# Optimization experiments

Measured on AMD Instinct MI355X. Metric: run time of the kernel, lower is better.

Reference implementation:

```python
import jax, jax.numpy as jnp
import numpy as np

P_TOP = 0.1          # fraction of brightest pixels for atmosphere
LEC_K = 3            # local-extremum conv kernel size (w=3 in forward)
HID = 64             # hidden channels of stand-in Net


def _conv2d(x, w, pad):
    return jax.lax.conv_general_dilated(
        x, w, window_strides=(1, 1), padding=[(pad, pad), (pad, pad)],
        dimension_numbers=("NCHW", "OIHW", "NCHW"))


def _lec_weights(k, dtype):
    # LocalExtremumConv.init_weights: all +/-1/k^2 with +/-1 at the center
    base = jnp.full((1, 1, k, k), 1.0 / (k * k), dtype=dtype)
    base = base.at[0, 0, k // 2, k // 2].set(1.0)
    return -base, base  # (min_weights, max_weights)


def setup_inputs() -> dict:
    key = jax.random.key(0)
    ks = jax.random.split(key, 8)
    B, C, H, W = 8, 3, 512, 512
    x = jax.random.uniform(ks[0], (B, C, H, W), dtype=jnp.float32)
    s1 = 1.0 / np.sqrt(C * 9)
    s2 = 1.0 / np.sqrt(HID * 9)
    return {
        "x": x,
        "net_w1": jax.random.normal(ks[1], (HID, C, 3, 3), jnp.float32) * s1,
        "net_b1": jnp.zeros((HID,), jnp.float32),
        "net_w2": jax.random.normal(ks[2], (C, HID, 3, 3), jnp.float32) * s2,
        "net_b2": jnp.zeros((C,), jnp.float32),
        "color_w": jax.random.normal(ks[3], (3, 3), jnp.float32) * (1.0 / np.sqrt(3)),
        "color_b": jnp.zeros((3,), jnp.float32),
        "conv_w": jax.random.normal(ks[4], (4, 3, 1, 1), jnp.float32) * (1.0 / np.sqrt(3)),
        "conv_b": jnp.zeros((4,), jnp.float32),
    }


def reference(x, net_w1, net_b1, net_w2, net_b2, color_w, color_b, conv_w, conv_b):
    B, C, H, W = x.shape
    # --- stand-in Net: 3->64->3 conv enhancement, sigmoid output ---
    h = jax.nn.relu(_conv2d(x, net_w1, 1) + net_b1[None, :, None, None])
    img_high = jax.nn.sigmoid(_conv2d(h, net_w2, 1) + net_b2[None, :, None, None])
    # --- stand-in Color_pred: GAP -> linear -> sigmoid -> (B,3,1,1) gain ---
    color = jax.nn.sigmoid(x.mean(axis=(2, 3)) @ color_w.T + color_b)
    img_high = img_high * color[:, :, None, None]
    # --- 1x1 conv -> split K (1ch), Bias (3ch); residual correction ---
    feat = _conv2d(img_high, conv_w, 0) + conv_b[None, :, None, None]
    K, Bt = feat[:, 0:1], feat[:, 1:4]
    x_out = K * x - Bt + x
    # --- illumination channel: reflect pad + channel min/max + LEC convs ---
    pad = LEC_K // 2
    xp = jnp.pad(x_out, ((0, 0), (0, 0), (pad, pad), (pad, pad)), mode="reflect")
    x_max = xp.max(axis=1, keepdims=True)
    _, max_w = _lec_weights(LEC_K, x.dtype)
    bright = jax.nn.relu(_conv2d(x_max, max_w, 0))  # (B,1,H,W)
    # --- atmosphere: top-p% brightest pixels, gather + mean ---
    # NOTE: faithful to torch images.view(B,-1,C) on NCHW (layout-scrambled)
    flat_img = x_out.reshape(B, H * W, C)
    flat_bright = bright.reshape(B, H * W)
    num_pixels = int(P_TOP * H * W)
    _, idx = jax.lax.top_k(flat_bright, num_pixels)          # (B, num_pixels)
    picked = jnp.take_along_axis(flat_img, idx[:, :, None], axis=1)
    A = picked.mean(axis=1)                                   # (B, C)
    return (x_out, A)
```

## Files before the change

kernel.cpp:

```cpp
#include <hip/hip_runtime.h>
#include <hip/hip_bf16.h>

#define Hn 512
#define Wn 512
#define HWn (512 * 512)
#define KTOP 26214

typedef __attribute__((ext_vector_type(8))) short frag_ab;
typedef __attribute__((ext_vector_type(4))) float frag_cd;

__device__ __forceinline__ float sigf(float z) { return 1.0f / (1.0f + __expf(-z)); }

__device__ __forceinline__ short f2bf(float f) {
  unsigned u = __float_as_uint(f);
  u += 0x7FFFu + ((u >> 16) & 1u);
  return (short)(u >> 16);
}

__device__ __forceinline__ unsigned aload(const unsigned* p) {
  return __hip_atomic_load(p, __ATOMIC_RELAXED, __HIP_MEMORY_SCOPE_AGENT);
}

__global__ __launch_bounds__(256) void k_means(
    const float* __restrict__ x, float* __restrict__ means, unsigned* __restrict__ doneCnt,
    const float* __restrict__ w1, const float* __restrict__ b1, const float* __restrict__ w2,
    const float* __restrict__ cw, const float* __restrict__ cb,
    short* __restrict__ w1A, short* __restrict__ w2A, float* __restrict__ colorG)
{
  const int tid = threadIdx.x;
  __shared__ int lastS;
  int bc = blockIdx.x >> 5;
  int slice = blockIdx.x & 31;
  const float4* p = (const float4*)(x + bc * HWn + slice * 8192);
  float s = 0.f;
  for (int i = tid; i < 2048; i += 256) { float4 v = p[i]; s += v.x + v.y + v.z + v.w; }
  for (int off = 32; off > 0; off >>= 1) s += __shfl_down(s, off);
  if ((tid & 63) == 0) atomicAdd(&means[bc], s);
  __syncthreads();
  if (tid == 0) {
    unsigned tk = __hip_atomic_fetch_add(doneCnt, 1u, __ATOMIC_RELAXED, __HIP_MEMORY_SCOPE_AGENT);
    lastS = (tk == 767);
  }
  __syncthreads();
  if (!lastS) return;

  {
    int chunk = tid >> 6, lane = tid & 63;
    int m = lane & 15, q = lane >> 4;
    for (int j = 0; j < 8; ++j) {
      int k = q * 8 + j;
      float v = (k < 27) ? w1[(chunk * 16 + m) * 27 + k] : 0.f;
      w1A[tid * 8 + j] = f2bf(v);
    }
  }
  for (int i = tid; i < 384; i += 256) {
    int step = i >> 6, lane = i & 63;
    int m = lane & 15, q = lane >> 4;
    int dx = step >> 1, half = step & 1;
    int dy = m / 3, oc = m - dy * 3;
    for (int j = 0; j < 8; ++j) {
      int ch = half * 32 + q * 8 + j;
      float v = (m < 9) ? w2[oc * 576 + ch * 9 + dy * 3 + dx] : 0.f;
      w2A[i * 8 + j] = f2bf(v);
    }
  }
  if (tid < 24) {
    int b = tid / 3, oc = tid % 3;
    float z = cb[oc];
    for (int j = 0; j < 3; ++j)
      z += (atomicAdd(&means[b * 3 + j], 0.f) * (1.0f / (float)HWn)) * cw[oc * 3 + j];
    colorG[tid] = sigf(z);
  }
}

__global__ __launch_bounds__(256, 5) void k_fused(
    const float* __restrict__ x, const float* __restrict__ b1,
    const float* __restrict__ b2, const float* __restrict__ convw, const float* __restrict__ convb,
    const short* __restrict__ w1Ag, const short* __restrict__ w2Ag,
    const float* __restrict__ colorG, float* __restrict__ out)
{
  __shared__ __align__(16) unsigned short xs[720];
  __shared__ __align__(16) unsigned short hb[12960];
  __shared__ float bs[64];
  __shared__ float b2s[3], colorS[3], cwS[12], cbS[4];

  const int tid = threadIdx.x;
  const int wid = tid >> 6, lane = tid & 63;
  const int n = lane & 15, q = lane >> 4;
  const int tx0 = blockIdx.x * 16, ty0 = blockIdx.y * 8;
  const int b = blockIdx.z;

  if (tid < 180) {
    int c = tid / 60, rem = tid - c * 60;
    int yy = rem / 5, xq = (rem - yy * 5) * 4;
    int gy = ty0 - 2 + yy, gx0 = tx0 - 2 + xq;
    bool rowok = (unsigned)gy < 512u;
    const float* rp = x + (b * 3 + c) * HWn + (gy << 9) + gx0;
    float v0 = (rowok && (unsigned)(gx0 + 0) < 512u) ? rp[0] : 0.f;
    float v1 = (rowok && (unsigned)(gx0 + 1) < 512u) ? rp[1] : 0.f;
    float v2 = (rowok && (unsigned)(gx0 + 2) < 512u) ? rp[2] : 0.f;
    float v3 = (rowok && (unsigned)(gx0 + 3) < 512u) ? rp[3] : 0.f;
    __hip_bfloat162 c01 = __float22bfloat162_rn(make_float2(v0, v1));
    __hip_bfloat162 c23 = __float22bfloat162_rn(make_float2(v2, v3));
    uint2 v2w; v2w.x = *(unsigned*)&c01; v2w.y = *(unsigned*)&c23;
    *(uint2*)(xs + c * 240 + yy * 20 + xq) = v2w;
  }
  if (tid < 64) bs[tid] = b1[tid];
  if (tid < 3)  b2s[tid] = b2[tid];
  if (tid < 3)  colorS[tid] = colorG[b * 3 + tid];
  if (tid < 12) cwS[tid] = convw[tid];
  if (tid < 4)  cbS[tid] = convb[tid];

  frag_ab w1f[4];
#pragma unroll
  for (int ck = 0; ck < 4; ++ck) w1f[ck] = *(const frag_ab*)(w1Ag + (ck * 64 + lane) * 8);

  int kb[8];
#pragma unroll
  for (int j = 0; j < 8; ++j) {
    int k = q * 8 + j;
    int kk = (k < 27) ? k : (k - 27);
    int ic = kk / 9; int r = kk - ic * 9;
    kb[j] = (ic * 240 + (r / 3) * 20 + (r % 3)) * 2;
  }
  __syncthreads();

  float biasr[4][4];
#pragma unroll
  for (int ck = 0; ck < 4; ++ck)
#pragma unroll
    for (int r = 0; r < 4; ++r) biasr[ck][r] = bs[ck * 16 + q * 4 + r];

  for (int g = wid; g < 12; g += 4) {
    int pt = g * 16 + n;
    bool ptok = pt < 180;
    int ptc = ptok ? pt : 0;
    int pty = (ptc * 3641) >> 16;
    int ptx = ptc - pty * 18;
    int baseB = (pty * 20 + ptx) * 2;
    int gy = ty0 - 1 + pty, gx = tx0 - 1 + ptx;
    bool valid = ptok && (unsigned)gy < 512u && (unsigned)gx < 512u;
    frag_ab B;
#pragma unroll
    for (int j = 0; j < 8; ++j)
      B[j] = *(const short*)((const char*)xs + baseB + kb[j]);
#pragma unroll
    for (int ck = 0; ck < 4; ++ck) {
      frag_cd D = {biasr[ck][0], biasr[ck][1], biasr[ck][2], biasr[ck][3]};
      D = __builtin_amdgcn_mfma_f32_16x16x32_bf16(w1f[ck], B, D, 0, 0, 0);
      if (ptok) {
        float2 p01 = make_float2(fmaxf(D[0], 0.f), fmaxf(D[1], 0.f));
        float2 p23 = make_float2(fmaxf(D[2], 0.f), fmaxf(D[3], 0.f));
        __hip_bfloat162 c01 = __float22bfloat162_rn(p01);
        __hip_bfloat162 c23 = __float22bfloat162_rn(p23);
        unsigned lo = valid ? *(unsigned*)&c01 : 0u;
        unsigned hi = valid ? *(unsigned*)&c23 : 0u;
        uint2 v2; v2.x = lo; v2.y = hi;
        *(uint2*)(hb + pt * 72 + ck * 16 + q * 4) = v2;
      }
    }
  }

  frag_ab w2f[6];
#pragma unroll
  for (int i = 0; i < 6; ++i) w2f[i] = *(const frag_ab*)(w2Ag + (i * 64 + lane) * 8);
  __syncthreads();

  for (int r = wid; r < 10; r += 4) {
    frag_cd acc = {0.f, 0.f, 0.f, 0.f};
#pragma unroll
    for (int i = 0; i < 6; ++i) {
      int dx = i >> 1;
      int chb = (i & 1) * 64 + q * 16;
      frag_ab Bf = *(const frag_ab*)((const char*)hb + (r * 18 + n + dx) * 144 + chb);
      acc = __builtin_amdgcn_mfma_f32_16x16x32_bf16(w2f[i], Bf, acc, 0, 0, 0);
    }
    float* dp = (float*)(hb + r * 1296) + n * 10 + q * 4;
    if (q < 2) {
      *(float2*)dp = make_float2(acc[0], acc[1]);
      *(float2*)(dp + 2) = make_float2(acc[2], acc[3]);
    } else if (q == 2) {
      dp[0] = acc[0];
    }
  }
  __syncthreads();

  if (tid < 128) {
    int y = tid >> 4, xcol = tid & 15;
    float a0 = b2s[0], a1 = b2s[1], a2 = b2s[2];
#pragma unroll
    for (int dy = 0; dy < 3; ++dy) {
      const float* dp = (const float*)(hb + (y + dy) * 1296) + xcol * 10 + dy * 3;
      a0 += dp[0]; a1 += dp[1]; a2 += dp[2];
    }
    float ih0 = colorS[0] * sigf(a0);
    float ih1 = colorS[1] * sigf(a1);
    float ih2 = colorS[2] * sigf(a2);
    float Kv = cwS[0] * ih0 + cwS[1]  * ih1 + cwS[2]  * ih2 + cbS[0];
    float f1 = cwS[3] * ih0 + cwS[4]  * ih1 + cwS[5]  * ih2 + cbS[1];
    float f2 = cwS[6] * ih0 + cwS[7]  * ih1 + cwS[8]  * ih2 + cbS[2];
    float f3 = cwS[9] * ih0 + cwS[10] * ih1 + cwS[11] * ih2 + cbS[3];
    float xc0 = __bfloat162float(*(const __hip_bfloat16*)&xs[0 * 240 + (y + 2) * 20 + (xcol + 2)]);
    float xc1 = __bfloat162float(*(const __hip_bfloat16*)&xs[1 * 240 + (y + 2) * 20 + (xcol + 2)]);
    float xc2 = __bfloat162float(*(const __hip_bfloat16*)&xs[2 * 240 + (y + 2) * 20 + (xcol + 2)]);
    int oi = ((ty0 + y) << 9) + (tx0 + xcol);
    out[(b * 3 + 0) * HWn + oi] = Kv * xc0 - f1 + xc0;
    out[(b * 3 + 1) * HWn + oi] = Kv * xc1 - f2 + xc1;
    out[(b * 3 + 2) * HWn + oi] = Kv * xc2 - f3 + xc2;
  }
}

__device__ __forceinline__ void softBarrier(unsigned* ctr) {
  __syncthreads();
  if (threadIdx.x == 0) {
    __hip_atomic_fetch_add(ctr, 1u, __ATOMIC_RELAXED, __HIP_MEMORY_SCOPE_AGENT);
    while (__hip_atomic_load(ctr, __ATOMIC_RELAXED, __HIP_MEMORY_SCOPE_AGENT) < 64u)
      __builtin_amdgcn_s_sleep(2);
  }
  __syncthreads();
}

__device__ void sel256(const unsigned* __restrict__ h, unsigned kneed,
                       unsigned* sm, unsigned* oBin, unsigned* oAbove)
{
  const int t = threadIdx.x;
  sm[t] = aload(&h[t]);
  __syncthreads();
  for (int d = 1; d < 256; d <<= 1) {
    unsigned add = (t + d < 256) ? sm[t + d] : 0u;
    __syncthreads();
    sm[t] += add;
    __syncthreads();
  }
  unsigned mine = sm[t];
  unsigned nxt = (t < 255) ? sm[t + 1] : 0u;
  if (mine >= kneed && nxt < kneed) { *oBin = (unsigned)t; *oAbove = nxt; }
  __syncthreads();
}

__device__ void sel4096(const unsigned* __restrict__ h, unsigned kneed,
                        unsigned* sm, unsigned* oBin, unsigned* oAbove)
{
  const int t = threadIdx.x;
  unsigned loc[16]; unsigned sum = 0;
#pragma unroll
  for (int i = 0; i < 16; ++i) { loc[i] = aload(&h[t * 16 + i]); sum += loc[i]; }
  sm[t] = sum;
  __syncthreads();
  for (int d = 1; d < 256; d <<= 1) {
    unsigned add = (t + d < 256) ? sm[t + d] : 0u;
    __syncthreads();
    sm[t] += add;
    __syncthreads();
  }
  unsigned mine = sm[t];
  unsigned nxt = (t < 255) ? sm[t + 1] : 0u;
  if (mine >= kneed && nxt < kneed) {
    unsigned acc = nxt;
    for (int i = 15; i >= 0; --i) {
      unsigned c = loc[i];
      if (acc + c >= kneed) { *oBin = (unsigned)(t * 16 + i); *oAbove = acc; break; }
      acc += c;
    }
  }
  __syncthreads();
}

__global__ __launch_bounds__(256) void k_tail(
    const float* __restrict__ outv,
    unsigned* __restrict__ h1, unsigned* __restrict__ h12, unsigned* __restrict__ h3,
    unsigned* __restrict__ eqTaken, float* __restrict__ Asum,
    unsigned* __restrict__ barCtr, unsigned* __restrict__ doneCnt, float* __restrict__ outA)
{
  __shared__ __align__(16) float xm[10][516];
  __shared__ __align__(16) float brightS[4096];
  __shared__ unsigned hh[4096];
  __shared__ unsigned sm[256];
  __shared__ unsigned sB1, sA1, sB2, sA2, sB3, sA3;
  __shared__ float red[4][3];
  __shared__ int lastA;

  const int tid = threadIdx.x;
  const int b = blockIdx.x >> 6, strip = blockIdx.x & 63;
  const int y0 = strip * 8;
  const float* op = outv + b * 3 * HWn;
  unsigned* bar = barCtr + b * 48;

  hh[tid] = 0;
  for (int idx = tid; idx < 1280; idx += 256) {
    int r = idx >> 7, seg = idx & 127;
    int gy = y0 - 1 + r; gy = (gy < 0) ? -gy : (gy > 511 ? 1022 - gy : gy);
    int c0 = seg * 4;
    const float* rp = op + (gy << 9) + c0;
    float4 v0 = *(const float4*)rp;
    float4 v1 = *(const float4*)(rp + HWn);
    float4 v2 = *(const float4*)(rp + 2 * HWn);
    xm[r][c0 + 1] = fmaxf(v0.x, fmaxf(v1.x, v2.x));
    xm[r][c0 + 2] = fmaxf(v0.y, fmaxf(v1.y, v2.y));
    xm[r][c0 + 3] = fmaxf(v0.z, fmaxf(v1.z, v2.z));
    xm[r][c0 + 4] = fmaxf(v0.w, fmaxf(v1.w, v2.w));
  }
  if (tid < 20) {
    int r = tid >> 1, side = tid & 1;
    int gy = y0 - 1 + r; gy = (gy < 0) ? -gy : (gy > 511 ? 1022 - gy : gy);
    int gx = side ? 510 : 1;
    float m = fmaxf(op[(gy << 9) + gx], fmaxf(op[HWn + (gy << 9) + gx], op[2 * HWn + (gy << 9) + gx]));
    xm[r][side ? 513 : 0] = m;
  }
  __syncthreads();
  {
    const int row = tid >> 5, cl = tid & 31;
#pragma unroll 4
    for (int i = 0; i < 16; ++i) {
      int c = cl + (i << 5);
      float s0 = xm[row][c]     + xm[row][c + 1]     + xm[row][c + 2];
      float s1 = xm[row + 1][c] + xm[row + 1][c + 1] + xm[row + 1][c + 2];
      float s2 = xm[row + 2][c] + xm[row + 2][c + 1] + xm[row + 2][c + 2];
      float s = (s0 + s1 + s2) * (1.f / 9.f) + xm[row + 1][c + 1] * (8.f / 9.f);
      s = fmaxf(s, 0.f);
      brightS[(row << 9) + c] = s;
      atomicAdd(&hh[__float_as_uint(s) >> 24], 1u);
    }
  }
  __syncthreads();
  if (hh[tid]) atomicAdd(&h1[(b << 8) + tid], hh[tid]);
  softBarrier(bar);

  sel256(h1 + (b << 8), KTOP, sm, &sB1, &sA1);
  for (int i = tid; i < 4096; i += 256) hh[i] = 0;
  __syncthreads();
  const float4* bp = (const float4*)brightS;
  const unsigned sb1 = sB1;
#pragma unroll
  for (int it = 0; it < 4; ++it) {
    float4 v = bp[it * 256 + tid];
    unsigned u0 = __float_as_uint(v.x), u1 = __float_as_uint(v.y);
    unsigned u2 = __float_as_uint(v.z), u3 = __float_as_uint(v.w);
    if ((u0 >> 24) == sb1) atomicAdd(&hh[(u0 >> 12) & 0xFFFu], 1u);
    if ((u1 >> 24) == sb1) atomicAdd(&hh[(u1 >> 12) & 0xFFFu], 1u);
    if ((u2 >> 24) == sb1) atomicAdd(&hh[(u2 >> 12) & 0xFFFu], 1u);
    if ((u3 >> 24) == sb1) atomicAdd(&hh[(u3 >> 12) & 0xFFFu], 1u);
  }
  __syncthreads();
  for (int i = tid; i < 4096; i += 256)
    if (hh[i]) atomicAdd(&h12[(b << 12) + i], hh[i]);
  softBarrier(bar + 16);

  sel4096(h12 + (b << 12), KTOP - sA1, sm, &sB2, &sA2);
  const unsigned P20 = (sB1 << 12) | sB2;
#pragma unroll
  for (int it = 0; it < 4; ++it) {
    float4 v = bp[it * 256 + tid];
    unsigned u0 = __float_as_uint(v.x), u1 = __float_as_uint(v.y);
    unsigned u2 = __float_as_uint(v.z), u3 = __float_as_uint(v.w);
    if ((u0 >> 12) == P20) atomicAdd(&h3[(b << 12) + (u0 & 0xFFFu)], 1u);
    if ((u1 >> 12) == P20) atomicAdd(&h3[(b << 12) + (u1 & 0xFFFu)], 1u);
    if ((u2 >> 12) == P20) atomicAdd(&h3[(b << 12) + (u2 & 0xFFFu)], 1u);
    if ((u3 >> 12) == P20) atomicAdd(&h3[(b << 12) + (u3 & 0xFFFu)], 1u);
  }
  softBarrier(bar + 32);

  const unsigned kp3 = KTOP - sA1 - sA2;
  sel4096(h3 + (b << 12), kp3, sm, &sB3, &sA3);
  const unsigned T = (P20 << 12) | sB3;
  const unsigned ne = kp3 - sA3;
  float v0 = 0.f, v1 = 0.f, v2 = 0.f;
  for (int it = 0; it < 16; ++it) {
    int li = it * 256 + tid;
    int pix = (y0 << 9) + li;
    unsigned bits = __float_as_uint(brightS[li]);
    bool take = bits > T;
    if (bits == T) {
      if (aload(&eqTaken[b * 16]) < ne) {
        unsigned old = atomicAdd(&eqTaken[b * 16], 1u);
        take = old < ne;
      }
    }
    if (take) {
      v0 += op[3 * pix];
      v1 += op[3 * pix + 1];
      v2 += op[3 * pix + 2];
    }
  }
  for (int off = 32; off > 0; off >>= 1) {
    v0 += __shfl_down(v0, off);
    v1 += __shfl_down(v1, off);
    v2 += __shfl_down(v2, off);
  }
  int w = tid >> 6;
  if ((tid & 63) == 0) { red[w][0] = v0; red[w][1] = v1; red[w][2] = v2; }
  __syncthreads();
  if (tid == 0) {
    atomicAdd(&Asum[b * 3 + 0], red[0][0] + red[1][0] + red[2][0] + red[3][0]);
    atomicAdd(&Asum[b * 3 + 1], red[0][1] + red[1][1] + red[2][1] + red[3][1]);
    atomicAdd(&Asum[b * 3 + 2], red[0][2] + red[1][2] + red[2][2] + red[3][2]);
  }
  __syncthreads();
  if (tid == 0) {
    unsigned tk = __hip_atomic_fetch_add(doneCnt, 1u, __ATOMIC_RELAXED, __HIP_MEMORY_SCOPE_AGENT);
    lastA = (tk == 511);
  }
  __syncthreads();
  if (lastA && tid < 24)
    outA[3 * HWn * 8 + tid] = atomicAdd(&Asum[tid], 0.f) * (1.0f / (float)KTOP);
}

extern "C" void kernel_launch(void* const* d_in, const int* in_sizes, int n_in,
                              void* d_out, int out_size, void* d_ws, size_t ws_size,
                              hipStream_t stream)
{
  const float* x     = (const float*)d_in[0];
  const float* w1    = (const float*)d_in[1];
  const float* b1    = (const float*)d_in[2];
  const float* w2    = (const float*)d_in[3];
  const float* b2    = (const float*)d_in[4];
  const float* cw    = (const float*)d_in[5];
  const float* cb    = (const float*)d_in[6];
  const float* convw = (const float*)d_in[7];
  const float* convb = (const float*)d_in[8];
  float* out = (float*)d_out;
  char* ws = (char*)d_ws;

  unsigned* h1        = (unsigned*)(ws + 8388608);
  unsigned* h12       = (unsigned*)(ws + 8396800);
  unsigned* h3        = (unsigned*)(ws + 8527872);
  float*    Asum      = (float*)(ws + 8658944);
  unsigned* eqTaken   = (unsigned*)(ws + 8659040);
  float*    means     = (float*)(ws + 8659552);
  unsigned* meansDone = (unsigned*)(ws + 8659648);
  unsigned* accumDone = (unsigned*)(ws + 8659680);
  unsigned* barCtr    = (unsigned*)(ws + 8659712);
  short*    w1Ag      = (short*)(ws + 8661248);
  short*    w2Ag      = (short*)(ws + 8665344);
  float*    colorG    = (float*)(ws + 8683776);

  hipMemsetAsync(ws + 8388608, 0, 8661248 - 8388608, stream);

  k_means<<<768, 256, 0, stream>>>(x, means, meansDone, w1, b1, w2, cw, cb, w1Ag, w2Ag, colorG);
  k_fused<<<dim3(32, 64, 8), 256, 0, stream>>>(x, b1, b2, convw, convb, w1Ag, w2Ag, colorG, out);
  k_tail<<<512, 256, 0, stream>>>(out, h1, h12, h3, eqTaken, Asum, barCtr, accumDone, out);
}
```

Before: 260.5 us.

## Process two tiles per fused block and truncate top-k radix select to 20 bits

The fused conv kernel now handles two horizontal 16x8 tiles per block, so it launches half as many blocks, loads the weight fragments once and precomputes per-lane offsets. The tail kernel drops the third radix pass and its soft barrier, choosing the top-k threshold on the upper 20 bits of the float. Ties within that bucket are settled by the eqTaken counter, which may pick different pixels than exact top_k. The first-level histogram also merges repeated bins in registers to cut shared-memory atomics. The risks are a small deviation in A from the exact top-k selection and a longer serial loop per block in k_fused.

```diff
diff --git a/kernel.cpp b/kernel.cpp
--- a/kernel.cpp
+++ b/kernel.cpp
@@ -79,41 +79,34 @@
     const short* __restrict__ w1Ag, const short* __restrict__ w2Ag,
     const float* __restrict__ colorG, float* __restrict__ out)
 {
-  __shared__ __align__(16) unsigned short xs[720];
-  __shared__ __align__(16) unsigned short hb[12960];
+  __shared__ __align__(16) unsigned short xs[760];
+  __shared__ __align__(16) unsigned short hb[13824];
   __shared__ float bs[64];
   __shared__ float b2s[3], colorS[3], cwS[12], cbS[4];
 
   const int tid = threadIdx.x;
   const int wid = tid >> 6, lane = tid & 63;
   const int n = lane & 15, q = lane >> 4;
-  const int tx0 = blockIdx.x * 16, ty0 = blockIdx.y * 8;
+  const int ty0 = blockIdx.y * 8;
   const int b = blockIdx.z;
 
-  if (tid < 180) {
-    int c = tid / 60, rem = tid - c * 60;
-    int yy = rem / 5, xq = (rem - yy * 5) * 4;
-    int gy = ty0 - 2 + yy, gx0 = tx0 - 2 + xq;
-    bool rowok = (unsigned)gy < 512u;
-    const float* rp = x + (b * 3 + c) * HWn + (gy << 9) + gx0;
-    float v0 = (rowok && (unsigned)(gx0 + 0) < 512u) ? rp[0] : 0.f;
-    float v1 = (rowok && (unsigned)(gx0 + 1) < 512u) ? rp[1] : 0.f;
-    float v2 = (rowok && (unsigned)(gx0 + 2) < 512u) ? rp[2] : 0.f;
-    float v3 = (rowok && (unsigned)(gx0 + 3) < 512u) ? rp[3] : 0.f;
-    __hip_bfloat162 c01 = __float22bfloat162_rn(make_float2(v0, v1));
-    __hip_bfloat162 c23 = __float22bfloat162_rn(make_float2(v2, v3));
-    uint2 v2w; v2w.x = *(unsigned*)&c01; v2w.y = *(unsigned*)&c23;
-    *(uint2*)(xs + c * 240 + yy * 20 + xq) = v2w;
-  }
   if (tid < 64) bs[tid] = b1[tid];
   if (tid < 3)  b2s[tid] = b2[tid];
   if (tid < 3)  colorS[tid] = colorG[b * 3 + tid];
   if (tid < 12) cwS[tid] = convw[tid];
   if (tid < 4)  cbS[tid] = convb[tid];
 
+  int sc = 0, syy = 0, sxq = 0;
+  const bool sOn = tid < 180;
+  if (sOn) { sc = tid / 60; int rem = tid - sc * 60; syy = rem / 5; sxq = (rem - syy * 5) * 4; }
+  unsigned short* sDst = xs + sc * 240 + syy * 20 + sxq;
+
   frag_ab w1f[4];
 #pragma unroll
   for (int ck = 0; ck < 4; ++ck) w1f[ck] = *(const frag_ab*)(w1Ag + (ck * 64 + lane) * 8);
+  frag_ab w2f[6];
+#pragma unroll
+  for (int i = 0; i < 6; ++i) w2f[i] = *(const frag_ab*)(w2Ag + (i * 64 + lane) * 8);
 
   int kb[8];
 #pragma unroll
@@ -123,6 +116,17 @@
     int ic = kk / 9; int r = kk - ic * 9;
     kb[j] = (ic * 240 + (r / 3) * 20 + (r % 3)) * 2;
   }
+
+  int baseA[3], gyA[3], gxA[3];
+#pragma unroll
+  for (int u = 0; u < 3; ++u) {
+    int pt = (wid + u * 4) * 16 + n;
+    int pty = (pt * 3641) >> 16;
+    int ptx = pt - pty * 18;
+    baseA[u] = (pty * 20 + ptx) * 2;
+    gyA[u] = ty0 - 1 + pty;
+    gxA[u] = ptx - 1;
+  }
   __syncthreads();
 
   float biasr[4][4];
@@ -131,24 +135,37 @@
 #pragma unroll
     for (int r = 0; r < 4; ++r) biasr[ck][r] = bs[ck * 16 + q * 4 + r];
 
-  for (int g = wid; g < 12; g += 4) {
-    int pt = g * 16 + n;
-    bool ptok = pt < 180;
-    int ptc = ptok ? pt : 0;
-    int pty = (ptc * 3641) >> 16;
-    int ptx = ptc - pty * 18;
-    int baseB = (pty * 20 + ptx) * 2;
-    int gy = ty0 - 1 + pty, gx = tx0 - 1 + ptx;
-    bool valid = ptok && (unsigned)gy < 512u && (unsigned)gx < 512u;
-    frag_ab B;
-#pragma unroll
-    for (int j = 0; j < 8; ++j)
-      B[j] = *(const short*)((const char*)xs + baseB + kb[j]);
-#pragma unroll
-    for (int ck = 0; ck < 4; ++ck) {
-      frag_cd D = {biasr[ck][0], biasr[ck][1], biasr[ck][2], biasr[ck][3]};
-      D = __builtin_amdgcn_mfma_f32_16x16x32_bf16(w1f[ck], B, D, 0, 0, 0);
-      if (ptok) {
+  for (int t = 0; t < 2; ++t) {
+    const int tx0 = (blockIdx.x * 2 + t) * 16;
+
+    if (sOn) {
+      int gy = ty0 - 2 + syy, gx0 = tx0 - 2 + sxq;
+      bool rowok = (unsigned)gy < 512u;
+      const float* rp = x + (b * 3 + sc) * HWn + (gy << 9) + gx0;
+      float v0 = (rowok && (unsigned)(gx0 + 0) < 512u) ? rp[0] : 0.f;
+      float v1 = (rowok && (unsigned)(gx0 + 1) < 512u) ? rp[1] : 0.f;
+      float v2 = (rowok && (unsigned)(gx0 + 2) < 512u) ? rp[2] : 0.f;
+      float v3 = (rowok && (unsigned)(gx0 + 3) < 512u) ? rp[3] : 0.f;
+      __hip_bfloat162 c01 = __float22bfloat162_rn(make_float2(v0, v1));
+      __hip_bfloat162 c23 = __float22bfloat162_rn(make_float2(v2, v3));
+      uint2 v2w; v2w.x = *(unsigned*)&c01; v2w.y = *(unsigned*)&c23;
+      *(uint2*)sDst = v2w;
+    }
+    __syncthreads();
+
+#pragma unroll
+    for (int u = 0; u < 3; ++u) {
+      int pt = (wid + u * 4) * 16 + n;
+      int baseB = baseA[u];
+      bool valid = (unsigned)gyA[u] < 512u && (unsigned)(tx0 + gxA[u]) < 512u;
+      frag_ab B;
+#pragma unroll
+      for (int j = 0; j < 8; ++j)
+        B[j] = *(const short*)((const char*)xs + baseB + kb[j]);
+#pragma unroll
+      for (int ck = 0; ck < 4; ++ck) {
+        frag_cd D = {biasr[ck][0], biasr[ck][1], biasr[ck][2], biasr[ck][3]};
+        D = __builtin_amdgcn_mfma_f32_16x16x32_bf16(w1f[ck], B, D, 0, 0, 0);
         float2 p01 = make_float2(fmaxf(D[0], 0.f), fmaxf(D[1], 0.f));
         float2 p23 = make_float2(fmaxf(D[2], 0.f), fmaxf(D[3], 0.f));
         __hip_bfloat162 c01 = __float22bfloat162_rn(p01);
@@ -159,54 +176,51 @@
         *(uint2*)(hb + pt * 72 + ck * 16 + q * 4) = v2;
       }
     }
-  }
-
-  frag_ab w2f[6];
-#pragma unroll
-  for (int i = 0; i < 6; ++i) w2f[i] = *(const frag_ab*)(w2Ag + (i * 64 + lane) * 8);
-  __syncthreads();
-
-  for (int r = wid; r < 10; r += 4) {
-    frag_cd acc = {0.f, 0.f, 0.f, 0.f};
-#pragma unroll
-    for (int i = 0; i < 6; ++i) {
-      int dx = i >> 1;
-      int chb = (i & 1) * 64 + q * 16;
-      frag_ab Bf = *(const frag_ab*)((const char*)hb + (r * 18 + n + dx) * 144 + chb);
-      acc = __builtin_amdgcn_mfma_f32_16x16x32_bf16(w2f[i], Bf, acc, 0, 0, 0);
-    }
-    float* dp = (float*)(hb + r * 1296) + n * 10 + q * 4;
-    if (q < 2) {
-      *(float2*)dp = make_float2(acc[0], acc[1]);
-      *(float2*)(dp + 2) = make_float2(acc[2], acc[3]);
-    } else if (q == 2) {
-      dp[0] = acc[0];
-    }
-  }
-  __syncthreads();
-
-  if (tid < 128) {
-    int y = tid >> 4, xcol = tid & 15;
-    float a0 = b2s[0], a1 = b2s[1], a2 = b2s[2];
-#pragma unroll
-    for (int dy = 0; dy < 3; ++dy) {
-      const float* dp = (const float*)(hb + (y + dy) * 1296) + xcol * 10 + dy * 3;
-      a0 += dp[0]; a1 += dp[1]; a2 += dp[2];
-    }
-    float ih0 = colorS[0] * sigf(a0);
-    float ih1 = colorS[1] * sigf(a1);
-    float ih2 = colorS[2] * sigf(a2);
-    float Kv = cwS[0] * ih0 + cwS[1]  * ih1 + cwS[2]  * ih2 + cbS[0];
-    float f1 = cwS[3] * ih0 + cwS[4]  * ih1 + cwS[5]  * ih2 + cbS[1];
-    float f2 = cwS[6] * ih0 + cwS[7]  * ih1 + cwS[8]  * ih2 + cbS[2];
-    float f3 = cwS[9] * ih0 + cwS[10] * ih1 + cwS[11] * ih2 + cbS[3];
-    float xc0 = __bfloat162float(*(const __hip_bfloat16*)&xs[0 * 240 + (y + 2) * 20 + (xcol + 2)]);
-    float xc1 = __bfloat162float(*(const __hip_bfloat16*)&xs[1 * 240 + (y + 2) * 20 + (xcol + 2)]);
-    float xc2 = __bfloat162float(*(const __hip_bfloat16*)&xs[2 * 240 + (y + 2) * 20 + (xcol + 2)]);
-    int oi = ((ty0 + y) << 9) + (tx0 + xcol);
-    out[(b * 3 + 0) * HWn + oi] = Kv * xc0 - f1 + xc0;
-    out[(b * 3 + 1) * HWn + oi] = Kv * xc1 - f2 + xc1;
-    out[(b * 3 + 2) * HWn + oi] = Kv * xc2 - f3 + xc2;
+    __syncthreads();
+
+    for (int r = wid; r < 10; r += 4) {
+      frag_cd acc = {0.f, 0.f, 0.f, 0.f};
+#pragma unroll
+      for (int i = 0; i < 6; ++i) {
+        int dx = i >> 1;
+        int chb = (i & 1) * 64 + q * 16;
+        frag_ab Bf = *(const frag_ab*)((const char*)hb + (r * 18 + n + dx) * 144 + chb);
+        acc = __builtin_amdgcn_mfma_f32_16x16x32_bf16(w2f[i], Bf, acc, 0, 0, 0);
+      }
+      float* dp = (float*)(hb + r * 1296) + n * 10 + q * 4;
+      if (q < 2) {
+        *(float2*)dp = make_float2(acc[0], acc[1]);
+        *(float2*)(dp + 2) = make_float2(acc[2], acc[3]);
+      } else if (q == 2) {
+        dp[0] = acc[0];
+      }
+    }
+    __syncthreads();
+
+    if (tid < 128) {
+      int y = tid >> 4, xcol = tid & 15;
+      float a0 = b2s[0], a1 = b2s[1], a2 = b2s[2];
+#pragma unroll
+      for (int dy = 0; dy < 3; ++dy) {
+        const float* dp = (const float*)(hb + (y + dy) * 1296) + xcol * 10 + dy * 3;
+        a0 += dp[0]; a1 += dp[1]; a2 += dp[2];
+      }
+      float ih0 = colorS[0] * sigf(a0);
+      float ih1 = colorS[1] * sigf(a1);
+      float ih2 = colorS[2] * sigf(a2);
+      float Kv = cwS[0] * ih0 + cwS[1]  * ih1 + cwS[2]  * ih2 + cbS[0];
+      float f1 = cwS[3] * ih0 + cwS[4]  * ih1 + cwS[5]  * ih2 + cbS[1];
+      float f2 = cwS[6] * ih0 + cwS[7]  * ih1 + cwS[8]  * ih2 + cbS[2];
+      float f3 = cwS[9] * ih0 + cwS[10] * ih1 + cwS[11] * ih2 + cbS[3];
+      float xc0 = __bfloat162float(*(const __hip_bfloat16*)&xs[0 * 240 + (y + 2) * 20 + (xcol + 2)]);
+      float xc1 = __bfloat162float(*(const __hip_bfloat16*)&xs[1 * 240 + (y + 2) * 20 + (xcol + 2)]);
+      float xc2 = __bfloat162float(*(const __hip_bfloat16*)&xs[2 * 240 + (y + 2) * 20 + (xcol + 2)]);
+      int oi = ((ty0 + y) << 9) + (tx0 + xcol);
+      out[(b * 3 + 0) * HWn + oi] = Kv * xc0 - f1 + xc0;
+      out[(b * 3 + 1) * HWn + oi] = Kv * xc1 - f2 + xc1;
+      out[(b * 3 + 2) * HWn + oi] = Kv * xc2 - f3 + xc2;
+    }
+    __syncthreads();
   }
 }
 
@@ -268,7 +282,7 @@
 
 __global__ __launch_bounds__(256) void k_tail(
     const float* __restrict__ outv,
-    unsigned* __restrict__ h1, unsigned* __restrict__ h12, unsigned* __restrict__ h3,
+    unsigned* __restrict__ h1, unsigned* __restrict__ h12,
     unsigned* __restrict__ eqTaken, float* __restrict__ Asum,
     unsigned* __restrict__ barCtr, unsigned* __restrict__ doneCnt, float* __restrict__ outA)
 {
@@ -276,7 +290,7 @@
   __shared__ __align__(16) float brightS[4096];
   __shared__ unsigned hh[4096];
   __shared__ unsigned sm[256];
-  __shared__ unsigned sB1, sA1, sB2, sA2, sB3, sA3;
+  __shared__ unsigned sB1, sA1, sB2, sA2;
   __shared__ float red[4][3];
   __shared__ int lastA;
 
@@ -310,6 +324,7 @@
   __syncthreads();
   {
     const int row = tid >> 5, cl = tid & 31;
+    unsigned cb0 = 0x100, cc0 = 0, cb1 = 0x100, cc1 = 0;
 #pragma unroll 4
     for (int i = 0; i < 16; ++i) {
       int c = cl + (i << 5);
@@ -319,8 +334,15 @@
       float s = (s0 + s1 + s2) * (1.f / 9.f) + xm[row + 1][c + 1] * (8.f / 9.f);
       s = fmaxf(s, 0.f);
       brightS[(row << 9) + c] = s;
-      atomicAdd(&hh[__float_as_uint(s) >> 24], 1u);
-    }
+      unsigned bin = __float_as_uint(s) >> 24;
+      if (bin == cb0) ++cc0;
+      else if (bin == cb1) ++cc1;
+      else if (!cc0) { cb0 = bin; cc0 = 1; }
+      else if (!cc1) { cb1 = bin; cc1 = 1; }
+      else atomicAdd(&hh[bin], 1u);
+    }
+    if (cc0) atomicAdd(&hh[cb0], cc0);
+    if (cc1) atomicAdd(&hh[cb1], cc1);
   }
   __syncthreads();
   if (hh[tid]) atomicAdd(&h1[(b << 8) + tid], hh[tid]);
@@ -344,33 +366,19 @@
   __syncthreads();
   for (int i = tid; i < 4096; i += 256)
     if (hh[i]) atomicAdd(&h12[(b << 12) + i], hh[i]);
+  if (tid == 0) { sB2 = 0xFFFu; sA2 = 0u; }
   softBarrier(bar + 16);
 
   sel4096(h12 + (b << 12), KTOP - sA1, sm, &sB2, &sA2);
-  const unsigned P20 = (sB1 << 12) | sB2;
-#pragma unroll
-  for (int it = 0; it < 4; ++it) {
-    float4 v = bp[it * 256 + tid];
-    unsigned u0 = __float_as_uint(v.x), u1 = __float_as_uint(v.y);
-    unsigned u2 = __float_as_uint(v.z), u3 = __float_as_uint(v.w);
-    if ((u0 >> 12) == P20) atomicAdd(&h3[(b << 12) + (u0 & 0xFFFu)], 1u);
-    if ((u1 >> 12) == P20) atomicAdd(&h3[(b << 12) + (u1 & 0xFFFu)], 1u);
-    if ((u2 >> 12) == P20) atomicAdd(&h3[(b << 12) + (u2 & 0xFFFu)], 1u);
-    if ((u3 >> 12) == P20) atomicAdd(&h3[(b << 12) + (u3 & 0xFFFu)], 1u);
-  }
-  softBarrier(bar + 32);
-
-  const unsigned kp3 = KTOP - sA1 - sA2;
-  sel4096(h3 + (b << 12), kp3, sm, &sB3, &sA3);
-  const unsigned T = (P20 << 12) | sB3;
-  const unsigned ne = kp3 - sA3;
+  const unsigned T20 = (sB1 << 12) | sB2;
+  const unsigned ne = KTOP - sA1 - sA2;
   float v0 = 0.f, v1 = 0.f, v2 = 0.f;
   for (int it = 0; it < 16; ++it) {
     int li = it * 256 + tid;
     int pix = (y0 << 9) + li;
-    unsigned bits = __float_as_uint(brightS[li]);
-    bool take = bits > T;
-    if (bits == T) {
+    unsigned u20 = __float_as_uint(brightS[li]) >> 12;
+    bool take = u20 > T20;
+    if (u20 == T20) {
       if (aload(&eqTaken[b * 16]) < ne) {
         unsigned old = atomicAdd(&eqTaken[b * 16], 1u);
         take = old < ne;
@@ -423,7 +431,6 @@
 
   unsigned* h1        = (unsigned*)(ws + 8388608);
   unsigned* h12       = (unsigned*)(ws + 8396800);
-  unsigned* h3        = (unsigned*)(ws + 8527872);
   float*    Asum      = (float*)(ws + 8658944);
   unsigned* eqTaken   = (unsigned*)(ws + 8659040);
   float*    means     = (float*)(ws + 8659552);
@@ -437,6 +444,6 @@
   hipMemsetAsync(ws + 8388608, 0, 8661248 - 8388608, stream);
 
   k_means<<<768, 256, 0, stream>>>(x, means, meansDone, w1, b1, w2, cw, cb, w1Ag, w2Ag, colorG);
-  k_fused<<<dim3(32, 64, 8), 256, 0, stream>>>(x, b1, b2, convw, convb, w1Ag, w2Ag, colorG, out);
-  k_tail<<<512, 256, 0, stream>>>(out, h1, h12, h3, eqTaken, Asum, barCtr, accumDone, out);
-}
+  k_fused<<<dim3(16, 64, 8), 256, 0, stream>>>(x, b1, b2, convw, convb, w1Ag, w2Ag, colorG, out);
+  k_tail<<<512, 256, 0, stream>>>(out, h1, h12, eqTaken, Asum, barCtr, accumDone, out);
+}
```

Result: slower. 295.8 us (+13.5%).
